# Optimization experiments

Hardware: AMD Instinct MI355X
Metric: run time of the kernel (lower is better)

The kernel has to match this reference:

```python
import jax, jax.numpy as jnp
import numpy as np


def setup_inputs() -> dict:
    key = jax.random.key(0)
    kx, kw = jax.random.split(key)
    x = jax.random.normal(kx, (2, 64, 16, 128, 128), dtype=jnp.float32)
    # Conv3d(in=2, out=1, kernel=7, padding=3, bias=False) weight, OIDHW layout
    w = jax.random.normal(kw, (1, 2, 7, 7, 7), dtype=jnp.float32) * (1.0 / np.sqrt(2 * 7 * 7 * 7))
    return {"x": x, "w": w}


def reference(x, w):
    # x: (B, C, T, H, W); w: (O=1, I=2, 7, 7, 7)
    max_out = jnp.max(x, axis=1, keepdims=True)   # (B,1,T,H,W)
    avg_out = jnp.mean(x, axis=1, keepdims=True)  # (B,1,T,H,W)
    concat = jnp.concatenate([max_out, avg_out], axis=1)  # (B,2,T,H,W)
    conv = jax.lax.conv_general_dilated(
        concat, w,
        window_strides=(1, 1, 1),
        padding=[(3, 3), (3, 3), (3, 3)],
        dimension_numbers=("NCDHW", "OIDHW", "NCDHW"),
    )  # (B,1,T,H,W)
    attn = jax.nn.sigmoid(conv)
    return attn * x
```

## Files before the change

kernel.cpp:

```cpp
#include <hip/hip_runtime.h>
#include <math.h>


#define NP (2 * 16 * 128 * 128)

typedef float vfloat4 __attribute__((ext_vector_type(4)));
typedef float vfloat2 __attribute__((ext_vector_type(2)));

__global__ __launch_bounds__(256) void pool_kernel(const float* __restrict__ x,
                                                   float* __restrict__ pmax,
                                                   float* __restrict__ pavg) {
    int j = blockIdx.x * 256 + threadIdx.x;
    int b = j >> 16;
    int rest = j & 65535;
    const float4* x4 = (const float4*)x;
    int base = (b << 22) | rest;

    float4 v = x4[base];
    float4 vmax = v;
    float4 vsum = v;
#pragma unroll 8
    for (int c = 1; c < 64; ++c) {
        float4 u = x4[base + (c << 16)];
        vmax.x = fmaxf(vmax.x, u.x);
        vmax.y = fmaxf(vmax.y, u.y);
        vmax.z = fmaxf(vmax.z, u.z);
        vmax.w = fmaxf(vmax.w, u.w);
        vsum.x += u.x; vsum.y += u.y; vsum.z += u.z; vsum.w += u.w;
    }
    const float s = 1.0f / 64.0f;
    float4 vavg; vavg.x = vsum.x * s; vavg.y = vsum.y * s; vavg.z = vsum.z * s; vavg.w = vsum.w * s;
    ((float4*)pmax)[j] = vmax;
    ((float4*)pavg)[j] = vavg;
}

__global__ __launch_bounds__(256) void conv_kernel(const float* __restrict__ pooled,
                                                   const float* __restrict__ wgt,
                                                   float* __restrict__ attn) {
    __shared__ __align__(16) float sm[2 * 38 * 40];

    int bid = blockIdx.x;
    int tw0 = (bid & 3) << 5;
    int th0 = ((bid >> 2) & 3) << 5;
    int t = (bid >> 4) & 15;
    int b = bid >> 8;

    int tid = threadIdx.x;
    int ty = tid >> 3;
    int txg = (tid & 7) << 2;

    float acc0 = 0.f, acc1 = 0.f, acc2 = 0.f, acc3 = 0.f;

    for (int dz = 0; dz < 7; ++dz) {
        int tsrc = t + dz - 3;
        if (tsrc < 0 || tsrc >= 16) continue;

        __syncthreads();
#pragma unroll
        for (int r = 0; r < 12; ++r) {
            int i = tid + (r << 8);
            int ch = i / 1444;
            int rem = i - ch * 1444;
            int y = rem / 38;
            int xx = rem - y * 38;
            int gh = th0 + y - 3;
            int gw = tw0 + xx - 3;
            float val = 0.f;
            if (i < 2888 && (unsigned)gh < 128u && (unsigned)gw < 128u)
                val = pooled[ch * NP + (((b << 4) + tsrc) << 14) + (gh << 7) + gw];
            if (i < 2888)
                sm[ch * 1520 + y * 40 + xx] = val;
        }
        __syncthreads();

        const float* wdz = wgt + dz * 49;
#pragma unroll
        for (int ch = 0; ch < 2; ++ch) {
#pragma unroll
            for (int dy = 0; dy < 7; ++dy) {
                const float* rp = &sm[ch * 1520 + (ty + dy) * 40 + txg];
                vfloat4 r0 = *(const vfloat4*)rp;
                vfloat4 r1 = *(const vfloat4*)(rp + 4);
                vfloat2 r2 = *(const vfloat2*)(rp + 8);
                float row[10] = {r0.x, r0.y, r0.z, r0.w,
                                 r1.x, r1.y, r1.z, r1.w,
                                 r2.x, r2.y};
                const float* wr = wdz + ch * 343 + dy * 7;
#pragma unroll
                for (int dx = 0; dx < 7; ++dx) {
                    float wv = wr[dx];
                    acc0 = fmaf(wv, row[dx + 0], acc0);
                    acc1 = fmaf(wv, row[dx + 1], acc1);
                    acc2 = fmaf(wv, row[dx + 2], acc2);
                    acc3 = fmaf(wv, row[dx + 3], acc3);
                }
            }
        }
    }

    vfloat4 av;
    av.x = 1.f / (1.f + __expf(-acc0));
    av.y = 1.f / (1.f + __expf(-acc1));
    av.z = 1.f / (1.f + __expf(-acc2));
    av.w = 1.f / (1.f + __expf(-acc3));

    int aidx = (((b << 4) + t) << 12) + ((th0 + ty) << 5) + ((tw0 + txg) >> 2);
    ((vfloat4*)attn)[aidx] = av;
}

__global__ __launch_bounds__(256) void mul_kernel(const float* __restrict__ x,
                                                  const float* __restrict__ attn,
                                                  float* __restrict__ out) {
    int g = blockIdx.x * 256 + threadIdx.x;
    int s = g & 65535;
    int c0 = g >> 16;
    const vfloat4* x4 = (const vfloat4*)x;
    const vfloat4* a4 = (const vfloat4*)attn;
    vfloat4* o4 = (vfloat4*)out;
#pragma unroll
    for (int b = 0; b < 2; ++b) {
        vfloat4 a = a4[(b << 16) | s];
        int base = (b << 22) | (c0 << 16) | s;
#pragma unroll
        for (int k = 0; k < 8; ++k) {
            int idx = base + (k << 19);
            __builtin_nontemporal_store(x4[idx] * a, &o4[idx]);
        }
    }
}

__global__ __launch_bounds__(256) void conv_mul_fused(const float* __restrict__ pooled,
                                                      const float* __restrict__ wgt,
                                                      const float* __restrict__ x,
                                                      float* __restrict__ out) {
    __shared__ float sm[2 * 38 * 39];

    int bid = blockIdx.x;
    int tw0 = (bid & 3) << 5;
    int th0 = ((bid >> 2) & 3) << 5;
    int t = (bid >> 4) & 15;
    int b = bid >> 8;

    int tid = threadIdx.x;
    int ty = tid >> 3;
    int txg = (tid & 7) << 2;

    int base4 = (b << 22) + (t << 12) + ((th0 + ty) << 5) + ((tw0 + txg) >> 2);
    int cs = bid & 63;
    const vfloat4* x4 = (const vfloat4*)x;
    vfloat4* o4 = (vfloat4*)out;

    vfloat4 pre[8];
#pragma unroll
    for (int k = 0; k < 8; ++k)
        pre[k] = x4[base4 + (((cs + k) & 63) << 16)];

    float acc0 = 0.f, acc1 = 0.f, acc2 = 0.f, acc3 = 0.f;

    for (int dz = 0; dz < 7; ++dz) {
        int tsrc = t + dz - 3;
        if (tsrc < 0 || tsrc >= 16) continue;

        __syncthreads();
        for (int i = tid; i < 2 * 38 * 38; i += 256) {
            int ch = i / 1444;
            int rem = i - ch * 1444;
            int y = rem / 38;
            int xx = rem - y * 38;
            int gh = th0 + y - 3;
            int gw = tw0 + xx - 3;
            float val = 0.f;
            if ((unsigned)gh < 128u && (unsigned)gw < 128u)
                val = pooled[ch * NP + (((b << 4) + tsrc) << 14) + (gh << 7) + gw];
            sm[ch * (38 * 39) + y * 39 + xx] = val;
        }
        __syncthreads();

        const float* wdz = wgt + dz * 49;
#pragma unroll
        for (int ch = 0; ch < 2; ++ch) {
#pragma unroll
            for (int dy = 0; dy < 7; ++dy) {
                const float* rp = &sm[ch * (38 * 39) + (ty + dy) * 39 + txg];
                float row[10];
#pragma unroll
                for (int k = 0; k < 10; ++k) row[k] = rp[k];
                const float* wr = wdz + ch * 343 + dy * 7;
#pragma unroll
                for (int dx = 0; dx < 7; ++dx) {
                    float wv = wr[dx];
                    acc0 = fmaf(wv, row[dx + 0], acc0);
                    acc1 = fmaf(wv, row[dx + 1], acc1);
                    acc2 = fmaf(wv, row[dx + 2], acc2);
                    acc3 = fmaf(wv, row[dx + 3], acc3);
                }
            }
        }
    }

    vfloat4 av;
    av.x = 1.f / (1.f + __expf(-acc0));
    av.y = 1.f / (1.f + __expf(-acc1));
    av.z = 1.f / (1.f + __expf(-acc2));
    av.w = 1.f / (1.f + __expf(-acc3));

#pragma unroll
    for (int k = 0; k < 8; ++k) {
        int idx = base4 + (((cs + k) & 63) << 16);
        __builtin_nontemporal_store(pre[k] * av, &o4[idx]);
    }
#pragma unroll 8
    for (int k = 8; k < 64; ++k) {
        int idx = base4 + (((cs + k) & 63) << 16);
        vfloat4 xv = x4[idx];
        __builtin_nontemporal_store(xv * av, &o4[idx]);
    }
}

extern "C" void kernel_launch(void* const* d_in, const int* in_sizes, int n_in,
                              void* d_out, int out_size, void* d_ws, size_t ws_size,
                              hipStream_t stream) {
    const float* x = (const float*)d_in[0];
    const float* w = (const float*)d_in[1];
    float* out = (float*)d_out;
    float* ws = (float*)d_ws;

    float* pmax = ws;
    float* pavg = ws + NP;

    pool_kernel<<<NP / 4 / 256, 256, 0, stream>>>(x, pmax, pavg);

    if (ws_size >= (size_t)(3 * NP) * sizeof(float)) {
        float* attn = ws + 2 * NP;
        conv_kernel<<<2 * 16 * 4 * 4, 256, 0, stream>>>(pmax, w, attn);
        mul_kernel<<<2048, 256, 0, stream>>>(x, attn, out);
    } else {
        conv_mul_fused<<<2 * 16 * 4 * 4, 256, 0, stream>>>(pmax, w, x, out);
    }
}
```

Before: 286.1 us.

## Fuse conv and broadcast multiply into one kernel with deeper x prefetch

```diff
diff --git a/kernel.cpp b/kernel.cpp
--- a/kernel.cpp
+++ b/kernel.cpp
@@ -34,9 +34,10 @@
     ((float4*)pavg)[j] = vavg;
 }
 
-__global__ __launch_bounds__(256) void conv_kernel(const float* __restrict__ pooled,
-                                                   const float* __restrict__ wgt,
-                                                   float* __restrict__ attn) {
+__global__ __launch_bounds__(256) void conv_mul_kernel(const float* __restrict__ pooled,
+                                                       const float* __restrict__ wgt,
+                                                       const float* __restrict__ x,
+                                                       float* __restrict__ out) {
     __shared__ __align__(16) float sm[2 * 38 * 40];
 
     int bid = blockIdx.x;
@@ -48,6 +49,16 @@
     int tid = threadIdx.x;
     int ty = tid >> 3;
     int txg = (tid & 7) << 2;
+
+    int base4 = (b << 22) + (t << 12) + ((th0 + ty) << 5) + ((tw0 + txg) >> 2);
+    int cs = bid & 63;
+    const vfloat4* x4 = (const vfloat4*)x;
+    vfloat4* o4 = (vfloat4*)out;
+
+    vfloat4 pre[16];
+#pragma unroll
+    for (int k = 0; k < 16; ++k)
+        pre[k] = x4[base4 + (((cs + k) & 63) << 16)];
 
     float acc0 = 0.f, acc1 = 0.f, acc2 = 0.f, acc3 = 0.f;
 
@@ -104,113 +115,13 @@
     av.z = 1.f / (1.f + __expf(-acc2));
     av.w = 1.f / (1.f + __expf(-acc3));
 
-    int aidx = (((b << 4) + t) << 12) + ((th0 + ty) << 5) + ((tw0 + txg) >> 2);
-    ((vfloat4*)attn)[aidx] = av;
-}
-
-__global__ __launch_bounds__(256) void mul_kernel(const float* __restrict__ x,
-                                                  const float* __restrict__ attn,
-                                                  float* __restrict__ out) {
-    int g = blockIdx.x * 256 + threadIdx.x;
-    int s = g & 65535;
-    int c0 = g >> 16;
-    const vfloat4* x4 = (const vfloat4*)x;
-    const vfloat4* a4 = (const vfloat4*)attn;
-    vfloat4* o4 = (vfloat4*)out;
 #pragma unroll
-    for (int b = 0; b < 2; ++b) {
-        vfloat4 a = a4[(b << 16) | s];
-        int base = (b << 22) | (c0 << 16) | s;
-#pragma unroll
-        for (int k = 0; k < 8; ++k) {
-            int idx = base + (k << 19);
-            __builtin_nontemporal_store(x4[idx] * a, &o4[idx]);
-        }
-    }
-}
-
-__global__ __launch_bounds__(256) void conv_mul_fused(const float* __restrict__ pooled,
-                                                      const float* __restrict__ wgt,
-                                                      const float* __restrict__ x,
-                                                      float* __restrict__ out) {
-    __shared__ float sm[2 * 38 * 39];
-
-    int bid = blockIdx.x;
-    int tw0 = (bid & 3) << 5;
-    int th0 = ((bid >> 2) & 3) << 5;
-    int t = (bid >> 4) & 15;
-    int b = bid >> 8;
-
-    int tid = threadIdx.x;
-    int ty = tid >> 3;
-    int txg = (tid & 7) << 2;
-
-    int base4 = (b << 22) + (t << 12) + ((th0 + ty) << 5) + ((tw0 + txg) >> 2);
-    int cs = bid & 63;
-    const vfloat4* x4 = (const vfloat4*)x;
-    vfloat4* o4 = (vfloat4*)out;
-
-    vfloat4 pre[8];
-#pragma unroll
-    for (int k = 0; k < 8; ++k)
-        pre[k] = x4[base4 + (((cs + k) & 63) << 16)];
-
-    float acc0 = 0.f, acc1 = 0.f, acc2 = 0.f, acc3 = 0.f;
-
-    for (int dz = 0; dz < 7; ++dz) {
-        int tsrc = t + dz - 3;
-        if (tsrc < 0 || tsrc >= 16) continue;
-
-        __syncthreads();
-        for (int i = tid; i < 2 * 38 * 38; i += 256) {
-            int ch = i / 1444;
-            int rem = i - ch * 1444;
-            int y = rem / 38;
-            int xx = rem - y * 38;
-            int gh = th0 + y - 3;
-            int gw = tw0 + xx - 3;
-            float val = 0.f;
-            if ((unsigned)gh < 128u && (unsigned)gw < 128u)
-                val = pooled[ch * NP + (((b << 4) + tsrc) << 14) + (gh << 7) + gw];
-            sm[ch * (38 * 39) + y * 39 + xx] = val;
-        }
-        __syncthreads();
-
-        const float* wdz = wgt + dz * 49;
-#pragma unroll
-        for (int ch = 0; ch < 2; ++ch) {
-#pragma unroll
-            for (int dy = 0; dy < 7; ++dy) {
-                const float* rp = &sm[ch * (38 * 39) + (ty + dy) * 39 + txg];
-                float row[10];
-#pragma unroll
-                for (int k = 0; k < 10; ++k) row[k] = rp[k];
-                const float* wr = wdz + ch * 343 + dy * 7;
-#pragma unroll
-                for (int dx = 0; dx < 7; ++dx) {
-                    float wv = wr[dx];
-                    acc0 = fmaf(wv, row[dx + 0], acc0);
-                    acc1 = fmaf(wv, row[dx + 1], acc1);
-                    acc2 = fmaf(wv, row[dx + 2], acc2);
-                    acc3 = fmaf(wv, row[dx + 3], acc3);
-                }
-            }
-        }
-    }
-
-    vfloat4 av;
-    av.x = 1.f / (1.f + __expf(-acc0));
-    av.y = 1.f / (1.f + __expf(-acc1));
-    av.z = 1.f / (1.f + __expf(-acc2));
-    av.w = 1.f / (1.f + __expf(-acc3));
-
-#pragma unroll
-    for (int k = 0; k < 8; ++k) {
+    for (int k = 0; k < 16; ++k) {
         int idx = base4 + (((cs + k) & 63) << 16);
         __builtin_nontemporal_store(pre[k] * av, &o4[idx]);
     }
 #pragma unroll 8
-    for (int k = 8; k < 64; ++k) {
+    for (int k = 16; k < 64; ++k) {
         int idx = base4 + (((cs + k) & 63) << 16);
         vfloat4 xv = x4[idx];
         __builtin_nontemporal_store(xv * av, &o4[idx]);
@@ -229,12 +140,5 @@
     float* pavg = ws + NP;
 
     pool_kernel<<<NP / 4 / 256, 256, 0, stream>>>(x, pmax, pavg);
-
-    if (ws_size >= (size_t)(3 * NP) * sizeof(float)) {
-        float* attn = ws + 2 * NP;
-        conv_kernel<<<2 * 16 * 4 * 4, 256, 0, stream>>>(pmax, w, attn);
-        mul_kernel<<<2048, 256, 0, stream>>>(x, attn, out);
-    } else {
-        conv_mul_fused<<<2 * 16 * 4 * 4, 256, 0, stream>>>(pmax, w, x, out);
-    }
+    conv_mul_kernel<<<2 * 16 * 4 * 4, 256, 0, stream>>>(pmax, w, x, out);
 }
```

Measured after the change: 266.7 us. 1.07x faster.

## Fuse pool, conv and multiply into one cooperative kernel with grid sync

Applied to the files above, without the earlier changes.

```diff
diff --git a/kernel.cpp b/kernel.cpp
--- a/kernel.cpp
+++ b/kernel.cpp
@@ -1,5 +1,8 @@
 #include <hip/hip_runtime.h>
+#include <hip/hip_cooperative_groups.h>
 #include <math.h>
+
+namespace cg = cooperative_groups;
 
 
 #define NP (2 * 16 * 128 * 128)
@@ -7,47 +10,60 @@
 typedef float vfloat4 __attribute__((ext_vector_type(4)));
 typedef float vfloat2 __attribute__((ext_vector_type(2)));
 
-__global__ __launch_bounds__(256) void pool_kernel(const float* __restrict__ x,
-                                                   float* __restrict__ pmax,
-                                                   float* __restrict__ pavg) {
-    int j = blockIdx.x * 256 + threadIdx.x;
-    int b = j >> 16;
-    int rest = j & 65535;
-    const float4* x4 = (const float4*)x;
-    int base = (b << 22) | rest;
-
-    float4 v = x4[base];
-    float4 vmax = v;
-    float4 vsum = v;
-#pragma unroll 8
-    for (int c = 1; c < 64; ++c) {
-        float4 u = x4[base + (c << 16)];
-        vmax.x = fmaxf(vmax.x, u.x);
-        vmax.y = fmaxf(vmax.y, u.y);
-        vmax.z = fmaxf(vmax.z, u.z);
-        vmax.w = fmaxf(vmax.w, u.w);
-        vsum.x += u.x; vsum.y += u.y; vsum.z += u.z; vsum.w += u.w;
-    }
-    const float s = 1.0f / 64.0f;
-    float4 vavg; vavg.x = vsum.x * s; vavg.y = vsum.y * s; vavg.z = vsum.z * s; vavg.w = vsum.w * s;
-    ((float4*)pmax)[j] = vmax;
-    ((float4*)pavg)[j] = vavg;
-}
-
-__global__ __launch_bounds__(256) void conv_kernel(const float* __restrict__ pooled,
-                                                   const float* __restrict__ wgt,
-                                                   float* __restrict__ attn) {
+__global__ __launch_bounds__(256) void fused_kernel(const float* __restrict__ x,
+                                                    const float* __restrict__ wgt,
+                                                    float* __restrict__ out,
+                                                    float* __restrict__ pooled) {
     __shared__ __align__(16) float sm[2 * 38 * 40];
 
+    int tid = threadIdx.x;
     int bid = blockIdx.x;
+
+    {
+        int j = bid * 256 + tid;
+        int jb = j >> 16;
+        int rest = j & 65535;
+        const float4* x4 = (const float4*)x;
+        int base = (jb << 22) | rest;
+
+        float4 v = x4[base];
+        float4 vmax = v;
+        float4 vsum = v;
+#pragma unroll 8
+        for (int c = 1; c < 64; ++c) {
+            float4 u = x4[base + (c << 16)];
+            vmax.x = fmaxf(vmax.x, u.x);
+            vmax.y = fmaxf(vmax.y, u.y);
+            vmax.z = fmaxf(vmax.z, u.z);
+            vmax.w = fmaxf(vmax.w, u.w);
+            vsum.x += u.x; vsum.y += u.y; vsum.z += u.z; vsum.w += u.w;
+        }
+        const float s = 1.0f / 64.0f;
+        float4 vavg; vavg.x = vsum.x * s; vavg.y = vsum.y * s; vavg.z = vsum.z * s; vavg.w = vsum.w * s;
+        ((float4*)pooled)[j] = vmax;
+        ((float4*)(pooled + NP))[j] = vavg;
+    }
+
+    __threadfence();
+    cg::this_grid().sync();
+
     int tw0 = (bid & 3) << 5;
     int th0 = ((bid >> 2) & 3) << 5;
     int t = (bid >> 4) & 15;
     int b = bid >> 8;
 
-    int tid = threadIdx.x;
     int ty = tid >> 3;
     int txg = (tid & 7) << 2;
+
+    int base4 = (b << 22) + (t << 12) + ((th0 + ty) << 5) + ((tw0 + txg) >> 2);
+    int cs = bid & 63;
+    const vfloat4* x4 = (const vfloat4*)x;
+    vfloat4* o4 = (vfloat4*)out;
+
+    vfloat4 pre[16];
+#pragma unroll
+    for (int k = 0; k < 16; ++k)
+        pre[k] = x4[base4 + (((cs + k) & 63) << 16)];
 
     float acc0 = 0.f, acc1 = 0.f, acc2 = 0.f, acc3 = 0.f;
 
@@ -104,36 +120,51 @@
     av.z = 1.f / (1.f + __expf(-acc2));
     av.w = 1.f / (1.f + __expf(-acc3));
 
-    int aidx = (((b << 4) + t) << 12) + ((th0 + ty) << 5) + ((tw0 + txg) >> 2);
-    ((vfloat4*)attn)[aidx] = av;
-}
-
-__global__ __launch_bounds__(256) void mul_kernel(const float* __restrict__ x,
-                                                  const float* __restrict__ attn,
-                                                  float* __restrict__ out) {
-    int g = blockIdx.x * 256 + threadIdx.x;
-    int s = g & 65535;
-    int c0 = g >> 16;
-    const vfloat4* x4 = (const vfloat4*)x;
-    const vfloat4* a4 = (const vfloat4*)attn;
-    vfloat4* o4 = (vfloat4*)out;
-#pragma unroll
-    for (int b = 0; b < 2; ++b) {
-        vfloat4 a = a4[(b << 16) | s];
-        int base = (b << 22) | (c0 << 16) | s;
-#pragma unroll
-        for (int k = 0; k < 8; ++k) {
-            int idx = base + (k << 19);
-            __builtin_nontemporal_store(x4[idx] * a, &o4[idx]);
-        }
-    }
-}
-
-__global__ __launch_bounds__(256) void conv_mul_fused(const float* __restrict__ pooled,
-                                                      const float* __restrict__ wgt,
-                                                      const float* __restrict__ x,
-                                                      float* __restrict__ out) {
-    __shared__ float sm[2 * 38 * 39];
+#pragma unroll
+    for (int k = 0; k < 16; ++k) {
+        int idx = base4 + (((cs + k) & 63) << 16);
+        __builtin_nontemporal_store(pre[k] * av, &o4[idx]);
+    }
+#pragma unroll 8
+    for (int k = 16; k < 64; ++k) {
+        int idx = base4 + (((cs + k) & 63) << 16);
+        vfloat4 xv = x4[idx];
+        __builtin_nontemporal_store(xv * av, &o4[idx]);
+    }
+}
+
+__global__ __launch_bounds__(256) void pool_kernel(const float* __restrict__ x,
+                                                   float* __restrict__ pmax,
+                                                   float* __restrict__ pavg) {
+    int j = blockIdx.x * 256 + threadIdx.x;
+    int b = j >> 16;
+    int rest = j & 65535;
+    const float4* x4 = (const float4*)x;
+    int base = (b << 22) | rest;
+
+    float4 v = x4[base];
+    float4 vmax = v;
+    float4 vsum = v;
+#pragma unroll 8
+    for (int c = 1; c < 64; ++c) {
+        float4 u = x4[base + (c << 16)];
+        vmax.x = fmaxf(vmax.x, u.x);
+        vmax.y = fmaxf(vmax.y, u.y);
+        vmax.z = fmaxf(vmax.z, u.z);
+        vmax.w = fmaxf(vmax.w, u.w);
+        vsum.x += u.x; vsum.y += u.y; vsum.z += u.z; vsum.w += u.w;
+    }
+    const float s = 1.0f / 64.0f;
+    float4 vavg; vavg.x = vsum.x * s; vavg.y = vsum.y * s; vavg.z = vsum.z * s; vavg.w = vsum.w * s;
+    ((float4*)pmax)[j] = vmax;
+    ((float4*)pavg)[j] = vavg;
+}
+
+__global__ __launch_bounds__(256) void conv_mul_kernel(const float* __restrict__ pooled,
+                                                       const float* __restrict__ wgt,
+                                                       const float* __restrict__ x,
+                                                       float* __restrict__ out) {
+    __shared__ __align__(16) float sm[2 * 38 * 40];
 
     int bid = blockIdx.x;
     int tw0 = (bid & 3) << 5;
@@ -150,9 +181,9 @@
     const vfloat4* x4 = (const vfloat4*)x;
     vfloat4* o4 = (vfloat4*)out;
 
-    vfloat4 pre[8];
-#pragma unroll
-    for (int k = 0; k < 8; ++k)
+    vfloat4 pre[16];
+#pragma unroll
+    for (int k = 0; k < 16; ++k)
         pre[k] = x4[base4 + (((cs + k) & 63) << 16)];
 
     float acc0 = 0.f, acc1 = 0.f, acc2 = 0.f, acc3 = 0.f;
@@ -162,7 +193,9 @@
         if (tsrc < 0 || tsrc >= 16) continue;
 
         __syncthreads();
-        for (int i = tid; i < 2 * 38 * 38; i += 256) {
+#pragma unroll
+        for (int r = 0; r < 12; ++r) {
+            int i = tid + (r << 8);
             int ch = i / 1444;
             int rem = i - ch * 1444;
             int y = rem / 38;
@@ -170,9 +203,10 @@
             int gh = th0 + y - 3;
             int gw = tw0 + xx - 3;
             float val = 0.f;
-            if ((unsigned)gh < 128u && (unsigned)gw < 128u)
+            if (i < 2888 && (unsigned)gh < 128u && (unsigned)gw < 128u)
                 val = pooled[ch * NP + (((b << 4) + tsrc) << 14) + (gh << 7) + gw];
-            sm[ch * (38 * 39) + y * 39 + xx] = val;
+            if (i < 2888)
+                sm[ch * 1520 + y * 40 + xx] = val;
         }
         __syncthreads();
 
@@ -181,10 +215,13 @@
         for (int ch = 0; ch < 2; ++ch) {
 #pragma unroll
             for (int dy = 0; dy < 7; ++dy) {
-                const float* rp = &sm[ch * (38 * 39) + (ty + dy) * 39 + txg];
-                float row[10];
-#pragma unroll
-                for (int k = 0; k < 10; ++k) row[k] = rp[k];
+                const float* rp = &sm[ch * 1520 + (ty + dy) * 40 + txg];
+                vfloat4 r0 = *(const vfloat4*)rp;
+                vfloat4 r1 = *(const vfloat4*)(rp + 4);
+                vfloat2 r2 = *(const vfloat2*)(rp + 8);
+                float row[10] = {r0.x, r0.y, r0.z, r0.w,
+                                 r1.x, r1.y, r1.z, r1.w,
+                                 r2.x, r2.y};
                 const float* wr = wdz + ch * 343 + dy * 7;
 #pragma unroll
                 for (int dx = 0; dx < 7; ++dx) {
@@ -205,12 +242,12 @@
     av.w = 1.f / (1.f + __expf(-acc3));
 
 #pragma unroll
-    for (int k = 0; k < 8; ++k) {
+    for (int k = 0; k < 16; ++k) {
         int idx = base4 + (((cs + k) & 63) << 16);
         __builtin_nontemporal_store(pre[k] * av, &o4[idx]);
     }
 #pragma unroll 8
-    for (int k = 8; k < 64; ++k) {
+    for (int k = 16; k < 64; ++k) {
         int idx = base4 + (((cs + k) & 63) << 16);
         vfloat4 xv = x4[idx];
         __builtin_nontemporal_store(xv * av, &o4[idx]);
@@ -227,14 +264,14 @@
 
     float* pmax = ws;
     float* pavg = ws + NP;
-
-    pool_kernel<<<NP / 4 / 256, 256, 0, stream>>>(x, pmax, pavg);
-
-    if (ws_size >= (size_t)(3 * NP) * sizeof(float)) {
-        float* attn = ws + 2 * NP;
-        conv_kernel<<<2 * 16 * 4 * 4, 256, 0, stream>>>(pmax, w, attn);
-        mul_kernel<<<2048, 256, 0, stream>>>(x, attn, out);
-    } else {
-        conv_mul_fused<<<2 * 16 * 4 * 4, 256, 0, stream>>>(pmax, w, x, out);
-    }
-}
+    (void)pavg;
+
+    void* args[] = {(void*)&x, (void*)&w, (void*)&out, (void*)&pmax};
+    hipError_t err = hipLaunchCooperativeKernel((void*)fused_kernel,
+                                                dim3(512), dim3(256),
+                                                args, 0, stream);
+    if (err != hipSuccess) {
+        pool_kernel<<<NP / 4 / 256, 256, 0, stream>>>(x, pmax, ws + NP);
+        conv_mul_kernel<<<2 * 16 * 4 * 4, 256, 0, stream>>>(pmax, w, x, out);
+    }
+}
```

After: 385.6 us. +34.8%, slower.
